# Performance work log

Hardware: AMD Instinct MI355X
Metric: run time of the kernel (lower is better)

The kernel has to match this reference:

```python
import jax, jax.numpy as jnp
import numpy as np

N = 400000      # total atoms
MAXD = 4        # max degree
NDEG = MAXD + 1 # degrees 0..4 (DeepChem min_degree=0)
F0 = 75         # ConvMolFeaturizer atom feature size
B = 16384       # number of graphs (batch_size)
NT = 12         # n_tasks
DIMS = [F0, 15, 20, 27, 36]


def setup_inputs() -> dict:
    key = jax.random.key(0)
    ks = jax.random.split(key, 40)
    inp = {}
    inp["atom_features"] = jax.random.normal(ks[0], (N, F0), jnp.float32)
    i = 1
    for l in range(4):
        fi, fo = DIMS[l], DIMS[l + 1]
        inp[f"Ws{l+1}"] = jax.random.normal(ks[i], (NDEG, fi, fo), jnp.float32) * 0.1; i += 1
        inp[f"Wn{l+1}"] = jax.random.normal(ks[i], (NDEG, fi, fo), jnp.float32) * 0.1; i += 1
        inp[f"b{l+1}"] = jax.random.normal(ks[i], (NDEG, fo), jnp.float32) * 0.1; i += 1
    inp["Wd2"] = jax.random.normal(ks[i], (2 * DIMS[-1], NT * 2), jnp.float32) * 0.1; i += 1
    inp["bd2"] = jnp.zeros((NT * 2,), jnp.float32)
    inp["Wl1"] = jax.random.normal(ks[i], (2 * NT, 96), jnp.float32) * 0.1; i += 1
    inp["bl1"] = jnp.zeros((96,), jnp.float32)
    inp["g1"] = jnp.ones((96,), jnp.float32)
    inp["be1"] = jnp.zeros((96,), jnp.float32)
    inp["Wl2"] = jax.random.normal(ks[i], (96, 63), jnp.float32) * 0.1; i += 1
    inp["bl2"] = jnp.zeros((63,), jnp.float32)
    inp["g2"] = jnp.ones((63,), jnp.float32)
    inp["be2"] = jnp.zeros((63,), jnp.float32)
    inp["Wl3"] = jax.random.normal(ks[i], (63, 138), jnp.float32) * 0.1; i += 1
    inp["bl3"] = jnp.zeros((138,), jnp.float32)
    inp["neighbor_list"] = jax.random.randint(ks[i], (N, MAXD), 0, N, dtype=jnp.int32); i += 1
    inp["degree"] = jax.random.randint(ks[i], (N,), 0, NDEG, dtype=jnp.int32); i += 1
    inp["membership"] = jnp.sort(jax.random.randint(ks[i], (N,), 0, B, dtype=jnp.int32)); i += 1
    inp["batch_size"] = B
    return inp


def _graph_conv(x, Ws, Wn, b, nbr, deg_onehot, nmask):
    # gather neighbor features and sum over (masked) neighbor slots: [N, Fin]
    nsum = (x[nbr] * nmask).sum(axis=1)
    # per-degree affine (DeepChem: separate self/neighbor weights per degree)
    pre = (jnp.einsum('nf,dfg->ndg', x, Ws)
           + jnp.einsum('nf,dfg->ndg', nsum, Wn)
           + b[None])                              # [N, NDEG, Fout]
    out = jnp.einsum('nd,ndg->ng', deg_onehot, pre)  # select row for atom's degree
    return jax.nn.selu(out)


def _bn(x, g, b, eps=1e-5):
    m = x.mean(axis=0)
    v = x.var(axis=0)
    return (x - m) * jax.lax.rsqrt(v + eps) * g + b


def reference(atom_features, Ws1, Wn1, b1, Ws2, Wn2, b2, Ws3, Wn3, b3,
              Ws4, Wn4, b4, Wd2, bd2, Wl1, bl1, g1, be1,
              Wl2, bl2, g2, be2, Wl3, bl3,
              neighbor_list, degree, membership, batch_size):
    deg_onehot = jax.nn.one_hot(degree, NDEG, dtype=atom_features.dtype)
    nmask = (jnp.arange(MAXD, dtype=degree.dtype)[None, :] < degree[:, None])
    nmask = nmask.astype(atom_features.dtype)[:, :, None]          # [N, MAXD, 1]

    x = _graph_conv(atom_features, Ws1, Wn1, b1, neighbor_list, deg_onehot, nmask)
    x = _graph_conv(x, Ws2, Wn2, b2, neighbor_list, deg_onehot, nmask)
    x = _graph_conv(x, Ws3, Wn3, b3, neighbor_list, deg_onehot, nmask)
    x = _graph_conv(x, Ws4, Wn4, b4, neighbor_list, deg_onehot, nmask)

    # GraphGather readout: concat(segment_sum, segment_max) then selu
    s = jax.ops.segment_sum(x, membership, num_segments=batch_size,
                            indices_are_sorted=True)
    m = jax.ops.segment_max(x, membership, num_segments=batch_size,
                            indices_are_sorted=True)
    m = jnp.where(jnp.isfinite(m), m, 0.0)  # empty graphs -> 0
    r = jax.nn.selu(jnp.concatenate([s, m], axis=1))               # [B, 72]

    logits = (r @ Wd2 + bd2).reshape(batch_size, -1, 2)            # [B, NT, 2]
    p = jax.nn.softmax(logits, axis=-1).reshape(batch_size, -1)    # [B, 2*NT]

    h = jax.nn.relu(_bn(p @ Wl1 + bl1, g1, be1))
    h = jax.nn.relu(_bn(h @ Wl2 + bl2, g2, be2))
    return jax.nn.sigmoid(h @ Wl3 + bl3)                            # [B, 138]
```

## Files before the change

### kernel.cpp

```cpp
#include <hip/hip_runtime.h>
#include <hip/hip_bf16.h>

#define N_ATOMS 400000
#define MAX_D   4
#define NDEG_   5
#define B_GR    16384
#define NTASK   12
#define AT      256
#define TA      64
#define NTHR    512
#define PADCAP  401408

__device__ __forceinline__ float selu_f(float x) {
    const float a = 1.6732632423543772f, s = 1.0507009873554805f;
    return x > 0.f ? s * x : s * a * (__expf(x) - 1.f);
}

__global__ void zero_kernel(int* ctr) {
    if (threadIdx.x < 10) ctr[threadIdx.x] = 0;
}

__launch_bounds__(256)
__global__ void fill_kernel(int* idx, int* degs_s, int4* nbrs_s, int4* nbro_s) {
    const int e = blockIdx.x * 256 + threadIdx.x;
    if (e < PADCAP) {
        idx[e] = -1;
        degs_s[e] = -1;
        nbrs_s[e] = make_int4(0, 0, 0, 0);
        nbro_s[e] = make_int4(0, 0, 0, 0);
    }
}

__launch_bounds__(256)
__global__ void hist_kernel(const int* __restrict__ deg, int* ctr) {
    __shared__ int h[NDEG_];
    if (threadIdx.x < NDEG_) h[threadIdx.x] = 0;
    __syncthreads();
    for (int i = blockIdx.x * 256 + threadIdx.x; i < N_ATOMS; i += gridDim.x * 256)
        atomicAdd(&h[deg[i]], 1);
    __syncthreads();
    if (threadIdx.x < NDEG_ && h[threadIdx.x]) atomicAdd(&ctr[threadIdx.x], h[threadIdx.x]);
}

__global__ void offsets_kernel(int* ctr) {
    if (threadIdx.x == 0) {
        int run = 0;
        for (int d = 0; d < NDEG_; ++d) {
            ctr[10 + d] = run;
            run += ctr[d];
            run = (run + AT - 1) & ~(AT - 1);
        }
        ctr[15] = run;
    }
}

__launch_bounds__(256)
__global__ void scatter_kernel(const int* __restrict__ deg, int* ctr,
                               int* idx, int* rank, int* degs_s) {
    __shared__ int h[NDEG_];
    __shared__ int base[NDEG_];
    const int i = blockIdx.x * 256 + threadIdx.x;
    const int d = (i < N_ATOMS) ? deg[i] : -1;
    if (threadIdx.x < NDEG_) h[threadIdx.x] = 0;
    __syncthreads();
    int intra = 0;
    if (i < N_ATOMS) intra = atomicAdd(&h[d], 1);
    __syncthreads();
    if (threadIdx.x < NDEG_ && h[threadIdx.x] > 0)
        base[threadIdx.x] = atomicAdd(&ctr[5 + threadIdx.x], h[threadIdx.x]);
    __syncthreads();
    if (i < N_ATOMS) {
        const int p = ctr[10 + d] + base[d] + intra;
        idx[p] = i;
        rank[i] = p;
        degs_s[p] = d;
    }
}

__launch_bounds__(256)
__global__ void nbrprep_kernel(const int* __restrict__ nbr, const int* __restrict__ rank,
                               int4* __restrict__ nbrs_s, int4* __restrict__ nbro_s) {
    const int i = blockIdx.x * 256 + threadIdx.x;
    if (i >= N_ATOMS) return;
    const int p = rank[i];
    const int4 nb = *reinterpret_cast<const int4*>(nbr + (size_t)i * MAX_D);
    nbro_s[p] = nb;
    nbrs_s[p] = make_int4(rank[nb.x], rank[nb.y], rank[nb.z], rank[nb.w]);
}

template<int FI, int FIP, int FO, bool FIRST, bool SCATTER_OUT, int DEG>
__device__ __forceinline__ void conv_body(const float* __restrict__ x,
                                          const float* __restrict__ Ws,
                                          const float* __restrict__ Wn,
                                          const float* __restrict__ bias,
                                          const int*   __restrict__ idx,
                                          float*       __restrict__ outs,
                                          float (*__restrict__ xt)[FIP],
                                          float (*__restrict__ nt)[FIP],
                                          const int*  s_a,
                                          const int4* s_nb,
                                          int pb, int tid)
{
    #pragma unroll 2
    for (int e = tid; e < TA * FI; e += NTHR) {
        const int al = e / FI, f = e - al * FI;
        const int4 nb = s_nb[al];
        const float xv = x[(size_t)s_a[al] * FI + f];
        float s = 0.f;
        if (DEG > 0) s += x[(size_t)nb.x * FI + f];
        if (DEG > 1) s += x[(size_t)nb.y * FI + f];
        if (DEG > 2) s += x[(size_t)nb.z * FI + f];
        if (DEG > 3) s += x[(size_t)nb.w * FI + f];
        xt[al][f] = xv;
        nt[al][f] = s;
    }
    __syncthreads();

    const int w = __builtin_amdgcn_readfirstlane(tid >> 6);
    const int l = tid & 63;
    constexpr int OPG = (FO + 7) / 8;
    const int o0 = w * OPG;
    const float* __restrict__ wsd = Ws + (DEG * FI) * FO + o0;
    const float* __restrict__ wnd = Wn + (DEG * FI) * FO + o0;
    const float* __restrict__ bb  = bias + DEG * FO + o0;

    float acc[OPG];
    #pragma unroll
    for (int oo = 0; oo < OPG; ++oo)
        acc[oo] = (o0 + oo < FO) ? bb[oo] : 0.f;

    for (int f = 0; f < FI; ++f) {
        const float xv = xt[l][f];
        const float nv = nt[l][f];
        const float* __restrict__ wsf = wsd + f * FO;
        const float* __restrict__ wnf = wnd + f * FO;
        #pragma unroll
        for (int oo = 0; oo < OPG; ++oo) {
            if (o0 + oo < FO)
                acc[oo] = fmaf(xv, wsf[oo], fmaf(nv, wnf[oo], acc[oo]));
        }
    }

    int row; bool store;
    if (SCATTER_OUT) { row = idx[pb + l]; store = (row >= 0); }
    else             { row = pb + l;      store = true; }
    if (store) {
        float* __restrict__ orow = outs + (size_t)row * FO + o0;
        #pragma unroll
        for (int oo = 0; oo < OPG; ++oo)
            if (o0 + oo < FO) orow[oo] = selu_f(acc[oo]);
    }
}

template<int FI, int FIP, int FO, bool FIRST, bool SCATTER_OUT>
__launch_bounds__(NTHR)
__global__ void conv_fused5(const float* __restrict__ x,
                            const int4*  __restrict__ nbr_,
                            const float* __restrict__ Ws,
                            const float* __restrict__ Wn,
                            const float* __restrict__ bias,
                            const int*   __restrict__ degs_s,
                            const int*   __restrict__ idx,
                            float*       __restrict__ outs)
{
    __shared__ float xt[TA][FIP];
    __shared__ float nt[TA][FIP];
    __shared__ int   s_a[TA];
    __shared__ int4  s_nb[TA];

    const int pb = blockIdx.x * TA;
    const int dfirst = degs_s[pb];
    if (dfirst < 0) return;
    const int tid = threadIdx.x;

    if (tid < TA) {
        const int p = pb + tid;
        int a = FIRST ? idx[p] : p;
        s_a[tid] = (a < 0) ? 0 : a;
        s_nb[tid] = nbr_[p];
    }
    __syncthreads();

    switch (__builtin_amdgcn_readfirstlane(dfirst)) {
    case 0: conv_body<FI, FIP, FO, FIRST, SCATTER_OUT, 0>(x, Ws, Wn, bias, idx, outs, xt, nt, s_a, s_nb, pb, tid); break;
    case 1: conv_body<FI, FIP, FO, FIRST, SCATTER_OUT, 1>(x, Ws, Wn, bias, idx, outs, xt, nt, s_a, s_nb, pb, tid); break;
    case 2: conv_body<FI, FIP, FO, FIRST, SCATTER_OUT, 2>(x, Ws, Wn, bias, idx, outs, xt, nt, s_a, s_nb, pb, tid); break;
    case 3: conv_body<FI, FIP, FO, FIRST, SCATTER_OUT, 3>(x, Ws, Wn, bias, idx, outs, xt, nt, s_a, s_nb, pb, tid); break;
    default: conv_body<FI, FIP, FO, FIRST, SCATTER_OUT, 4>(x, Ws, Wn, bias, idx, outs, xt, nt, s_a, s_nb, pb, tid); break;
    }
}

__launch_bounds__(64)
__global__ void readout_kernel(const float* __restrict__ x4o,
                               const int*   __restrict__ mem,
                               const float* __restrict__ Wd2,
                               const float* __restrict__ bd2,
                               float*       __restrict__ p)
{
    const int g = blockIdx.x;
    const int t = threadIdx.x;

    int lo = 0, hi = N_ATOMS;
    while (lo < hi) { int mid = (lo + hi) >> 1; if (mem[mid] < g) lo = mid + 1; else hi = mid; }
    int lo2 = lo, hi2 = N_ATOMS;
    while (lo2 < hi2) { int mid = (lo2 + hi2) >> 1; if (mem[mid] < g + 1) lo2 = mid + 1; else hi2 = mid; }

    __shared__ float r[72];
    if (t < 36) {
        float s = 0.f, m = -3.4e38f;
        for (int a = lo; a < lo2; ++a) {
            float v = x4o[(size_t)a * 36 + t];
            s += v;
            m = fmaxf(m, v);
        }
        if (lo2 == lo) m = 0.f;
        r[t]      = selu_f(s);
        r[36 + t] = selu_f(m);
    }
    __syncthreads();
    if (t < 24) {
        float acc = bd2[t];
        #pragma unroll
        for (int f = 0; f < 72; ++f) acc += r[f] * Wd2[f * 24 + t];
        float part = __shfl_xor(acc, 1);
        p[g * 24 + t] = 1.f / (1.f + __expf(part - acc));
    }
}

__launch_bounds__(256)
__global__ void dense1_kernel(const float* __restrict__ p,
                              const float* __restrict__ Wl1,
                              const float* __restrict__ bl1,
                              float*       __restrict__ y1)
{
    const int idx = blockIdx.x * 256 + threadIdx.x;
    if (idx >= B_GR * 96) return;
    const int row = idx / 96, c = idx - row * 96;
    float acc = bl1[c];
    const float* pr = p + row * 24;
    #pragma unroll
    for (int f = 0; f < 24; ++f) acc += pr[f] * Wl1[f * 96 + c];
    y1[idx] = acc;
}

template<int C>
__launch_bounds__(256)
__global__ void stats_kernel(const float* __restrict__ y, float* __restrict__ st)
{
    const int c = blockIdx.x;
    float s = 0.f, q = 0.f;
    for (int r = threadIdx.x; r < B_GR; r += 256) {
        const float v = y[r * C + c];
        s += v; q += v * v;
    }
    __shared__ float ss[256], qq[256];
    ss[threadIdx.x] = s; qq[threadIdx.x] = q;
    __syncthreads();
    for (int off = 128; off > 0; off >>= 1) {
        if (threadIdx.x < off) {
            ss[threadIdx.x] += ss[threadIdx.x + off];
            qq[threadIdx.x] += qq[threadIdx.x + off];
        }
        __syncthreads();
    }
    if (threadIdx.x == 0) {
        const float mean = ss[0] / (float)B_GR;
        const float var  = qq[0] / (float)B_GR - mean * mean;
        st[c]     = mean;
        st[C + c] = rsqrtf(var + 1e-5f);
    }
}

__launch_bounds__(256)
__global__ void dense2_kernel(const float* __restrict__ y1,
                              const float* __restrict__ st1,
                              const float* __restrict__ g1,
                              const float* __restrict__ be1,
                              const float* __restrict__ Wl2,
                              const float* __restrict__ bl2,
                              float*       __restrict__ y2)
{
    __shared__ float h[4 * 96];
    const int r0 = blockIdx.x * 4;
    for (int e = threadIdx.x; e < 4 * 96; e += 256) {
        const int rr = e / 96, c = e - rr * 96;
        float v = y1[(r0 + rr) * 96 + c];
        v = (v - st1[c]) * st1[96 + c] * g1[c] + be1[c];
        h[e] = fmaxf(v, 0.f);
    }
    __syncthreads();
    for (int e = threadIdx.x; e < 4 * 63; e += 256) {
        const int rr = e / 63, o = e - rr * 63;
        float acc = bl2[o];
        #pragma unroll
        for (int f = 0; f < 96; ++f) acc += h[rr * 96 + f] * Wl2[f * 63 + o];
        y2[(r0 + rr) * 63 + o] = acc;
    }
}

__launch_bounds__(320)
__global__ void dense3_kernel(const float* __restrict__ y2,
                              const float* __restrict__ st2,
                              const float* __restrict__ g2,
                              const float* __restrict__ be2,
                              const float* __restrict__ Wl3,
                              const float* __restrict__ bl3,
                              float*       __restrict__ out)
{
    __shared__ float h[2 * 63];
    const int r0 = blockIdx.x * 2;
    for (int e = threadIdx.x; e < 2 * 63; e += 320) {
        const int rr = e / 63, c = e - rr * 63;
        float v = y2[(r0 + rr) * 63 + c];
        v = (v - st2[c]) * st2[63 + c] * g2[c] + be2[c];
        h[e] = fmaxf(v, 0.f);
    }
    __syncthreads();
    for (int e = threadIdx.x; e < 2 * 138; e += 320) {
        const int rr = e / 138, o = e - rr * 138;
        float acc = bl3[o];
        #pragma unroll
        for (int f = 0; f < 63; ++f) acc += h[rr * 63 + f] * Wl3[f * 138 + o];
        out[(r0 + rr) * 138 + o] = 1.f / (1.f + __expf(-acc));
    }
}

extern "C" void kernel_launch(void* const* d_in, const int* in_sizes, int n_in,
                              void* d_out, int out_size, void* d_ws, size_t ws_size,
                              hipStream_t stream)
{
    (void)in_sizes; (void)n_in; (void)out_size; (void)ws_size;

    const float* af  = (const float*)d_in[0];
    const float* Ws1 = (const float*)d_in[1];
    const float* Wn1 = (const float*)d_in[2];
    const float* b1  = (const float*)d_in[3];
    const float* Ws2 = (const float*)d_in[4];
    const float* Wn2 = (const float*)d_in[5];
    const float* b2  = (const float*)d_in[6];
    const float* Ws3 = (const float*)d_in[7];
    const float* Wn3 = (const float*)d_in[8];
    const float* b3  = (const float*)d_in[9];
    const float* Ws4 = (const float*)d_in[10];
    const float* Wn4 = (const float*)d_in[11];
    const float* b4  = (const float*)d_in[12];
    const float* Wd2 = (const float*)d_in[13];
    const float* bd2 = (const float*)d_in[14];
    const float* Wl1 = (const float*)d_in[15];
    const float* bl1 = (const float*)d_in[16];
    const float* g1  = (const float*)d_in[17];
    const float* be1 = (const float*)d_in[18];
    const float* Wl2 = (const float*)d_in[19];
    const float* bl2 = (const float*)d_in[20];
    const float* g2  = (const float*)d_in[21];
    const float* be2 = (const float*)d_in[22];
    const float* Wl3 = (const float*)d_in[23];
    const float* bl3 = (const float*)d_in[24];
    const int*   nbr = (const int*)d_in[25];
    const int*   deg = (const int*)d_in[26];
    const int*   mem = (const int*)d_in[27];

    float* ws = (float*)d_ws;
    float* A = ws;
    float* B = A + (size_t)PADCAP * 27;
    int*   idx    = (int*)(B + (size_t)PADCAP * 36);
    int*   rank   = idx + PADCAP;
    int*   degs_s = rank + N_ATOMS;
    int4*  nbrs_s = (int4*)(degs_s + PADCAP);
    int4*  nbro_s = nbrs_s + PADCAP;
    int*   ctr    = (int*)(nbro_s + PADCAP);

    float* x1  = A;
    float* x2  = B;
    float* x3  = A;
    float* x4o = B;
    float* p   = A;
    float* y1  = A + 393216;
    float* y2  = A + 393216 + 1572864;
    float* st1 = A + 393216 + 1572864 + 1032192;
    float* st2 = st1 + 192;

    zero_kernel<<<1, 16, 0, stream>>>(ctr);
    fill_kernel<<<PADCAP / 256, 256, 0, stream>>>(idx, degs_s, nbrs_s, nbro_s);
    hist_kernel<<<1024, 256, 0, stream>>>(deg, ctr);
    offsets_kernel<<<1, 1, 0, stream>>>(ctr);
    scatter_kernel<<<(N_ATOMS + 255) / 256, 256, 0, stream>>>(deg, ctr, idx, rank, degs_s);
    nbrprep_kernel<<<(N_ATOMS + 255) / 256, 256, 0, stream>>>(nbr, rank, nbrs_s, nbro_s);

    conv_fused5<75, 77, 15, true,  false><<<PADCAP / TA, NTHR, 0, stream>>>
        (af, nbro_s, Ws1, Wn1, b1, degs_s, idx, x1);
    conv_fused5<15, 17, 20, false, false><<<PADCAP / TA, NTHR, 0, stream>>>
        (x1, nbrs_s, Ws2, Wn2, b2, degs_s, idx, x2);
    conv_fused5<20, 21, 27, false, false><<<PADCAP / TA, NTHR, 0, stream>>>
        (x2, nbrs_s, Ws3, Wn3, b3, degs_s, idx, x3);
    conv_fused5<27, 29, 36, false, true ><<<PADCAP / TA, NTHR, 0, stream>>>
        (x3, nbrs_s, Ws4, Wn4, b4, degs_s, idx, x4o);

    readout_kernel<<<B_GR, 64, 0, stream>>>(x4o, mem, Wd2, bd2, p);

    dense1_kernel<<<(B_GR * 96) / 256, 256, 0, stream>>>(p, Wl1, bl1, y1);
    stats_kernel<96><<<96, 256, 0, stream>>>(y1, st1);
    dense2_kernel<<<B_GR / 4, 256, 0, stream>>>(y1, st1, g1, be1, Wl2, bl2, y2);
    stats_kernel<63><<<63, 256, 0, stream>>>(y2, st2);
    dense3_kernel<<<B_GR / 2, 320, 0, stream>>>(y2, st2, g2, be2, Wl3, bl3, (float*)d_out);
}
```

Measured before the change: 653.3 us.

## Split first graph conv into per-atom projection and bf16 neighbor-sum combine

The first layer previously gathered four 75-wide raw feature rows per atom. It now projects each atom once through all four degree-specific neighbor weights and its own self weight. The neighbor projections are stored as 15-wide bf16 rows per degree, so the combine kernel gathers only small projected rows and sums them. This reorders the matmul and the neighbor sum by linearity to cut gather traffic from the wide input. In exchange it does four extra neighbor-weight matmuls per atom, adds an intermediate buffer with a second launch, and rounds the neighbor terms to bf16.

```diff
diff --git a/kernel.cpp b/kernel.cpp
--- a/kernel.cpp
+++ b/kernel.cpp
@@ -11,9 +11,19 @@
 #define NTHR    512
 #define PADCAP  401408
 
+typedef float float4u __attribute__((ext_vector_type(4), aligned(4)));
+
 __device__ __forceinline__ float selu_f(float x) {
     const float a = 1.6732632423543772f, s = 1.0507009873554805f;
     return x > 0.f ? s * x : s * a * (__expf(x) - 1.f);
+}
+
+__device__ __forceinline__ unsigned short f2bf(float x) {
+    unsigned int u = __float_as_uint(x);
+    return (unsigned short)((u + 0x7FFFu + ((u >> 16) & 1u)) >> 16);
+}
+__device__ __forceinline__ float bf2f(unsigned int s) {
+    return __uint_as_float(s << 16);
 }
 
 __global__ void zero_kernel(int* ctr) {
@@ -88,7 +98,154 @@
     nbrs_s[p] = make_int4(rank[nb.x], rank[nb.y], rank[nb.z], rank[nb.w]);
 }
 
-template<int FI, int FIP, int FO, bool FIRST, bool SCATTER_OUT, int DEG>
+__launch_bounds__(NTHR)
+__global__ void conv1_project(const float* __restrict__ af,
+                              const float* __restrict__ Ws1,
+                              const float* __restrict__ Wn1,
+                              const float* __restrict__ b1,
+                              const int*   __restrict__ degs_s,
+                              const int*   __restrict__ idx,
+                              float*       __restrict__ S,
+                              unsigned short* __restrict__ Z)
+{
+    __shared__ float xt[TA][76];
+    __shared__ int s_a[TA];
+
+    const int pb = blockIdx.x * TA;
+    const int dfirst = degs_s[pb];
+    if (dfirst < 0) return;
+    const int tid = threadIdx.x;
+
+    if (tid < TA) {
+        int a = idx[pb + tid];
+        s_a[tid] = (a < 0) ? 0 : a;
+    }
+    __syncthreads();
+
+    #pragma unroll 2
+    for (int e = tid; e < TA * 18; e += NTHR) {
+        const int al = e / 18, f4 = e - al * 18;
+        *(float4u*)&xt[al][f4 * 4] = *(const float4u*)(af + (size_t)s_a[al] * 75 + f4 * 4);
+    }
+    for (int e = tid; e < TA * 3; e += NTHR) {
+        const int al = e / 3, r = e - al * 3;
+        xt[al][72 + r] = af[(size_t)s_a[al] * 75 + 72 + r];
+    }
+    __syncthreads();
+
+    const int w = __builtin_amdgcn_readfirstlane(tid >> 6);
+    const int l = tid & 63;
+
+    if (w < 4) {
+        const float* __restrict__ wn = Wn1 + (size_t)(w + 1) * 75 * 15;
+        float acc[15];
+        #pragma unroll
+        for (int o = 0; o < 15; ++o) acc[o] = 0.f;
+        for (int f4 = 0; f4 < 18; ++f4) {
+            const float4u xv = *(const float4u*)&xt[l][f4 * 4];
+            #pragma unroll
+            for (int k = 0; k < 4; ++k) {
+                const float* __restrict__ wf = wn + (f4 * 4 + k) * 15;
+                #pragma unroll
+                for (int o = 0; o < 15; ++o) acc[o] = fmaf(xv[k], wf[o], acc[o]);
+            }
+        }
+        #pragma unroll
+        for (int k = 0; k < 3; ++k) {
+            const float xv = xt[l][72 + k];
+            const float* __restrict__ wf = wn + (72 + k) * 15;
+            #pragma unroll
+            for (int o = 0; o < 15; ++o) acc[o] = fmaf(xv, wf[o], acc[o]);
+        }
+        unsigned short zr[16];
+        #pragma unroll
+        for (int o = 0; o < 15; ++o) zr[o] = f2bf(acc[o]);
+        zr[15] = 0;
+        unsigned short* zp = Z + ((size_t)w * PADCAP + pb + l) * 16;
+        ((int4*)zp)[0] = ((const int4*)zr)[0];
+        ((int4*)zp)[1] = ((const int4*)zr)[1];
+    } else {
+        const int o0 = (w - 4) * 4;
+        const int d = __builtin_amdgcn_readfirstlane(dfirst);
+        const float* __restrict__ wsp = Ws1 + (size_t)d * 75 * 15 + o0;
+        const float* __restrict__ bb  = b1 + d * 15 + o0;
+        float acc[4];
+        #pragma unroll
+        for (int oo = 0; oo < 4; ++oo) acc[oo] = (o0 + oo < 15) ? bb[oo] : 0.f;
+        for (int f4 = 0; f4 < 18; ++f4) {
+            const float4u xv = *(const float4u*)&xt[l][f4 * 4];
+            #pragma unroll
+            for (int k = 0; k < 4; ++k) {
+                const float* __restrict__ wf = wsp + (f4 * 4 + k) * 15;
+                #pragma unroll
+                for (int oo = 0; oo < 4; ++oo)
+                    if (o0 + oo < 15) acc[oo] = fmaf(xv[k], wf[oo], acc[oo]);
+            }
+        }
+        #pragma unroll
+        for (int k = 0; k < 3; ++k) {
+            const float xv = xt[l][72 + k];
+            const float* __restrict__ wf = wsp + (72 + k) * 15;
+            #pragma unroll
+            for (int oo = 0; oo < 4; ++oo)
+                if (o0 + oo < 15) acc[oo] = fmaf(xv, wf[oo], acc[oo]);
+        }
+        float4u sv = {acc[0], acc[1], acc[2], acc[3]};
+        *(float4u*)(S + (size_t)(pb + l) * 16 + o0) = sv;
+    }
+}
+
+template<int DEG>
+__device__ __forceinline__ void combine_body(const float* __restrict__ S,
+                                             const unsigned short* __restrict__ Z,
+                                             const int4* __restrict__ nbrs_s,
+                                             float* __restrict__ x1, int p)
+{
+    float acc[16];
+    #pragma unroll
+    for (int q = 0; q < 4; ++q)
+        *(float4u*)&acc[q * 4] = *(const float4u*)(S + (size_t)p * 16 + q * 4);
+
+    if (DEG > 0) {
+        const int4 nb = nbrs_s[p];
+        const int nbid[4] = {nb.x, nb.y, nb.z, nb.w};
+        #pragma unroll
+        for (int j = 0; j < DEG; ++j) {
+            const unsigned short* zp = Z + ((size_t)(DEG - 1) * PADCAP + nbid[j]) * 16;
+            unsigned int zz[8];
+            *(int4*)&zz[0] = ((const int4*)zp)[0];
+            *(int4*)&zz[4] = ((const int4*)zp)[1];
+            #pragma unroll
+            for (int o = 0; o < 15; ++o)
+                acc[o] += bf2f((zz[o >> 1] >> ((o & 1) * 16)) & 0xffffu);
+        }
+    }
+    #pragma unroll
+    for (int o = 0; o < 15; ++o)
+        x1[(size_t)p * 15 + o] = selu_f(acc[o]);
+}
+
+__launch_bounds__(256)
+__global__ void conv1_combine(const float* __restrict__ S,
+                              const unsigned short* __restrict__ Z,
+                              const int4* __restrict__ nbrs_s,
+                              const int*  __restrict__ degs_s,
+                              float*      __restrict__ x1)
+{
+    const int base = blockIdx.x * 256;
+    const int dfirst = degs_s[base];
+    if (dfirst < 0) return;
+    const int p = base + threadIdx.x;
+    switch (__builtin_amdgcn_readfirstlane(dfirst)) {
+    case 0: combine_body<0>(S, Z, nbrs_s, x1, p); break;
+    case 1: combine_body<1>(S, Z, nbrs_s, x1, p); break;
+    case 2: combine_body<2>(S, Z, nbrs_s, x1, p); break;
+    case 3: combine_body<3>(S, Z, nbrs_s, x1, p); break;
+    default: combine_body<4>(S, Z, nbrs_s, x1, p); break;
+    }
+}
+
+template<int FI, int FIP, int FO, bool SCATTER_OUT, int DEG>
 __device__ __forceinline__ void conv_body(const float* __restrict__ x,
                                           const float* __restrict__ Ws,
                                           const float* __restrict__ Wn,
@@ -152,7 +309,7 @@
     }
 }
 
-template<int FI, int FIP, int FO, bool FIRST, bool SCATTER_OUT>
+template<int FI, int FIP, int FO, bool SCATTER_OUT>
 __launch_bounds__(NTHR)
 __global__ void conv_fused5(const float* __restrict__ x,
                             const int4*  __restrict__ nbr_,
@@ -175,18 +332,17 @@
 
     if (tid < TA) {
         const int p = pb + tid;
-        int a = FIRST ? idx[p] : p;
-        s_a[tid] = (a < 0) ? 0 : a;
+        s_a[tid] = p;
         s_nb[tid] = nbr_[p];
     }
     __syncthreads();
 
     switch (__builtin_amdgcn_readfirstlane(dfirst)) {
-    case 0: conv_body<FI, FIP, FO, FIRST, SCATTER_OUT, 0>(x, Ws, Wn, bias, idx, outs, xt, nt, s_a, s_nb, pb, tid); break;
-    case 1: conv_body<FI, FIP, FO, FIRST, SCATTER_OUT, 1>(x, Ws, Wn, bias, idx, outs, xt, nt, s_a, s_nb, pb, tid); break;
-    case 2: conv_body<FI, FIP, FO, FIRST, SCATTER_OUT, 2>(x, Ws, Wn, bias, idx, outs, xt, nt, s_a, s_nb, pb, tid); break;
-    case 3: conv_body<FI, FIP, FO, FIRST, SCATTER_OUT, 3>(x, Ws, Wn, bias, idx, outs, xt, nt, s_a, s_nb, pb, tid); break;
-    default: conv_body<FI, FIP, FO, FIRST, SCATTER_OUT, 4>(x, Ws, Wn, bias, idx, outs, xt, nt, s_a, s_nb, pb, tid); break;
+    case 0: conv_body<FI, FIP, FO, SCATTER_OUT, 0>(x, Ws, Wn, bias, idx, outs, xt, nt, s_a, s_nb, pb, tid); break;
+    case 1: conv_body<FI, FIP, FO, SCATTER_OUT, 1>(x, Ws, Wn, bias, idx, outs, xt, nt, s_a, s_nb, pb, tid); break;
+    case 2: conv_body<FI, FIP, FO, SCATTER_OUT, 2>(x, Ws, Wn, bias, idx, outs, xt, nt, s_a, s_nb, pb, tid); break;
+    case 3: conv_body<FI, FIP, FO, SCATTER_OUT, 3>(x, Ws, Wn, bias, idx, outs, xt, nt, s_a, s_nb, pb, tid); break;
+    default: conv_body<FI, FIP, FO, SCATTER_OUT, 4>(x, Ws, Wn, bias, idx, outs, xt, nt, s_a, s_nb, pb, tid); break;
     }
 }
 
@@ -363,7 +519,8 @@
     float* ws = (float*)d_ws;
     float* A = ws;
     float* B = A + (size_t)PADCAP * 27;
-    int*   idx    = (int*)(B + (size_t)PADCAP * 36);
+    float* Zr = B + (size_t)PADCAP * 36;
+    int*   idx    = (int*)(Zr + (size_t)PADCAP * 32);
     int*   rank   = idx + PADCAP;
     int*   degs_s = rank + N_ATOMS;
     int4*  nbrs_s = (int4*)(degs_s + PADCAP);
@@ -371,6 +528,8 @@
     int*   ctr    = (int*)(nbro_s + PADCAP);
 
     float* x1  = A;
+    float* Sb  = B;
+    unsigned short* Zb = (unsigned short*)Zr;
     float* x2  = B;
     float* x3  = A;
     float* x4o = B;
@@ -387,13 +546,14 @@
     scatter_kernel<<<(N_ATOMS + 255) / 256, 256, 0, stream>>>(deg, ctr, idx, rank, degs_s);
     nbrprep_kernel<<<(N_ATOMS + 255) / 256, 256, 0, stream>>>(nbr, rank, nbrs_s, nbro_s);
 
-    conv_fused5<75, 77, 15, true,  false><<<PADCAP / TA, NTHR, 0, stream>>>
-        (af, nbro_s, Ws1, Wn1, b1, degs_s, idx, x1);
-    conv_fused5<15, 17, 20, false, false><<<PADCAP / TA, NTHR, 0, stream>>>
+    conv1_project<<<PADCAP / TA, NTHR, 0, stream>>>(af, Ws1, Wn1, b1, degs_s, idx, Sb, Zb);
+    conv1_combine<<<PADCAP / 256, 256, 0, stream>>>(Sb, Zb, nbrs_s, degs_s, x1);
+
+    conv_fused5<15, 17, 20, false><<<PADCAP / TA, NTHR, 0, stream>>>
         (x1, nbrs_s, Ws2, Wn2, b2, degs_s, idx, x2);
-    conv_fused5<20, 21, 27, false, false><<<PADCAP / TA, NTHR, 0, stream>>>
+    conv_fused5<20, 21, 27, false><<<PADCAP / TA, NTHR, 0, stream>>>
         (x2, nbrs_s, Ws3, Wn3, b3, degs_s, idx, x3);
-    conv_fused5<27, 29, 36, false, true ><<<PADCAP / TA, NTHR, 0, stream>>>
+    conv_fused5<27, 29, 36, true ><<<PADCAP / TA, NTHR, 0, stream>>>
         (x3, nbrs_s, Ws4, Wn4, b4, degs_s, idx, x4o);
 
     readout_kernel<<<B_GR, 64, 0, stream>>>(x4o, mem, Wd2, bd2, p);
```

Measured after the change: 710.8 us. 8.8% more time.
